# Optimization experiments

Measured on AMD Instinct MI355X. Metric: run time of the kernel, lower is better.

## Reference

```python
import jax, jax.numpy as jnp
import numpy as np

B, T, C = 2, 2048, 1024
N_HEADS = 16
HEAD_DIM = C // N_HEADS

def setup_inputs() -> dict:
    key = jax.random.key(0)
    k1, k2, k3 = jax.random.split(key, 3)
    x = jax.random.normal(k1, (B, T, C), dtype=jnp.float32)
    W_qkv = jax.random.normal(k2, (C, 3 * C), dtype=jnp.float32) * (1.0 / np.sqrt(C))
    W_out = jax.random.normal(k3, (C, C), dtype=jnp.float32) * (1.0 / np.sqrt(C))
    return {"x": x, "W_qkv": W_qkv, "W_out": W_out}

def reference(x, W_qkv, W_out):
    b, t, c = x.shape
    qkv = jnp.einsum('btc,cd->btd', x, W_qkv)  # [B,T,3C]
    q, k, v = jnp.split(qkv, 3, axis=-1)
    # [B, H, T, hd]
    q = q.reshape(b, t, N_HEADS, HEAD_DIM).transpose(0, 2, 1, 3)
    k = k.reshape(b, t, N_HEADS, HEAD_DIM).transpose(0, 2, 1, 3)
    v = v.reshape(b, t, N_HEADS, HEAD_DIM).transpose(0, 2, 1, 3)
    scale = 1.0 / jnp.sqrt(jnp.asarray(HEAD_DIM, dtype=x.dtype))
    attn = jnp.einsum('bhqd,bhkd->bhqk', q, k) * scale  # [B,H,T,T]
    causal = jnp.tril(jnp.ones((t, t), dtype=bool))
    attn = jnp.where(causal, attn, jnp.asarray(-1e9, dtype=attn.dtype))
    attn = jax.nn.softmax(attn, axis=-1)
    out = jnp.einsum('bhqk,bhkd->bhqd', attn, v)
    out = out.transpose(0, 2, 1, 3).reshape(b, t, c)
    return jnp.einsum('btc,cd->btd', out, W_out)
```

## Files before the change

### kernel.cpp

```cpp
#include <hip/hip_runtime.h>
#include <hip/hip_bf16.h>

typedef __attribute__((ext_vector_type(8))) short short8;
typedef __attribute__((ext_vector_type(4))) short bf16x4;
typedef __attribute__((ext_vector_type(4))) float floatx4;

#define T_SEQ 2048
#define NH    16
#define HD    64
#define QSCALE 0.18033688f

#define MFMA16(a, b, c) __builtin_amdgcn_mfma_f32_16x16x16bf16_1k(a, b, c, 0, 0, 0)
#define MFMA32(a, b, c) __builtin_amdgcn_mfma_f32_16x16x32_bf16(a, b, c, 0, 0, 0)

__device__ __forceinline__ ushort f2bf(float f) {
    union { float f; unsigned u; } un; un.f = f;
    unsigned r = un.u + 0x7fff + ((un.u >> 16) & 1);
    return (ushort)(r >> 16);
}
__device__ __forceinline__ unsigned pkbf(float a, float b) {
    __hip_bfloat162 t = __float22bfloat162_rn(float2{a, b});
    return *reinterpret_cast<unsigned*>(&t);
}

typedef const __attribute__((address_space(1))) unsigned int* gp1_t;
typedef __attribute__((address_space(3))) unsigned int* lp3_t;
__device__ __forceinline__ void gl_lds16(const ushort* g, ushort* l) {
    __builtin_amdgcn_global_load_lds((gp1_t)g, (lp3_t)l, 16, 0, 0);
}

__global__ void prep_kernel(const float* __restrict__ Wqkv, const float* __restrict__ Wout,
                            const float* __restrict__ x, ushort* __restrict__ wt_qkv,
                            ushort* __restrict__ wt_out, ushort* __restrict__ x_bf) {
    __shared__ ushort tile[32][33];
    const int bid = blockIdx.x;
    if (bid >= 4096) {
        size_t i = ((size_t)(bid - 4096) * 256 + threadIdx.x) * 8;
        float4 f0 = *(const float4*)(x + i);
        float4 f1 = *(const float4*)(x + i + 4);
        short8 v;
        v[0] = (short)f2bf(f0.x); v[1] = (short)f2bf(f0.y);
        v[2] = (short)f2bf(f0.z); v[3] = (short)f2bf(f0.w);
        v[4] = (short)f2bf(f1.x); v[5] = (short)f2bf(f1.y);
        v[6] = (short)f2bf(f1.z); v[7] = (short)f2bf(f1.w);
        *(short8*)(x_bf + i) = v;
        return;
    }
    const float* in; ushort* out; int R, C, gx, gy;
    if (bid < 3072) { in = Wqkv; out = wt_qkv; R = 1024; C = 3072; gx = bid % 96; gy = bid / 96; }
    else            { int t = bid - 3072; in = Wout; out = wt_out; R = 1024; C = 1024; gx = t & 31; gy = t >> 5; }
    const int tx = threadIdx.x & 31, ty = threadIdx.x >> 5;
    const int bx = gx * 32, by = gy * 32;
    #pragma unroll
    for (int i = ty; i < 32; i += 8)
        tile[i][tx] = f2bf(in[(size_t)(by + i) * C + bx + tx]);
    __syncthreads();
    #pragma unroll
    for (int i = ty; i < 32; i += 8)
        out[(size_t)(bx + i) * R + by + tx] = tile[tx][i];
}

template <int EPI, int BN, int CM, int CN>
__global__ __launch_bounds__(256, 3)
void gemm_bt(const ushort* __restrict__ A, const ushort* __restrict__ Bt,
             void* __restrict__ O0, ushort* __restrict__ O1, ushort* __restrict__ O2,
             int M, int N, int K) {
    constexpr int NJ = BN / 32;
    constexpr int NB = (BN * 8) / 256;
    __shared__ __align__(16) ushort smem[8192 + BN * 64];
    ushort* As = smem;
    ushort* Bs = smem + 8192;
    const int tid  = threadIdx.x;
    const int wave = tid >> 6, lane = tid & 63;
    const int quad = lane >> 4, l16 = lane & 15;
    const int wm = (wave >> 1) * 64, wn = (wave & 1) * (BN / 2);

    const int lid = blockIdx.y * gridDim.x + blockIdx.x;
    const int xcd = lid & 7, ib = lid >> 3;
    const int NGY = (int)gridDim.y / CN;
    const int m0 = ((xcd / NGY) * CM + ib / CN) * 128;
    const int n0 = ((xcd % NGY) * CN + ib % CN) * BN;

    const ushort* aP[4];
    const ushort* bP[NB];
    #pragma unroll
    for (int j = 0; j < 4; j++) {
        int c = tid + j * 256;
        int r = c >> 3;
        int g = ((c & 7) ^ (r & 7)) * 8;
        aP[j] = A + (size_t)(m0 + r) * K + g;
    }
    #pragma unroll
    for (int j = 0; j < NB; j++) {
        int c = tid + j * 256;
        int r = c >> 3;
        int g = ((c & 7) ^ (r & 7)) * 8;
        bP[j] = Bt + (size_t)(n0 + r) * K + g;
    }

    floatx4 acc[4][NJ];
    #pragma unroll
    for (int i = 0; i < 4; i++)
        #pragma unroll
        for (int j = 0; j < NJ; j++)
            acc[i][j] = (floatx4){0.f, 0.f, 0.f, 0.f};

    const int xsw = l16 & 7;

    for (int k0 = 0; k0 < K; k0 += 64) {
        __syncthreads();
        #pragma unroll
        for (int j = 0; j < 4; j++)  gl_lds16(aP[j] + k0, &As[(tid + j * 256) * 8]);
        #pragma unroll
        for (int j = 0; j < NB; j++) gl_lds16(bP[j] + k0, &Bs[(tid + j * 256) * 8]);
        __syncthreads();
        #pragma unroll
        for (int kk = 0; kk < 2; kk++) {
            short8 af[4], bf[NJ];
            #pragma unroll
            for (int i = 0; i < 4; i++)
                af[i] = *(const short8*)(&As[(wm + i * 16 + l16) * 64 + ((kk * 4 + quad) ^ xsw) * 8]);
            #pragma unroll
            for (int j = 0; j < NJ; j++)
                bf[j] = *(const short8*)(&Bs[(wn + j * 16 + l16) * 64 + ((kk * 4 + quad) ^ xsw) * 8]);
            #pragma unroll
            for (int i = 0; i < 4; i++)
                #pragma unroll
                for (int j = 0; j < NJ; j++)
                    acc[i][j] = MFMA32(af[i], bf[j], acc[i][j]);
        }
    }

    if constexpr (EPI == 0) {
        const int b = m0 >> 11;
        const int t0 = m0 & 2047;
        if (n0 >= 2048) {
            const int head0 = (n0 - 2048) >> 6;
            __syncthreads();
            #pragma unroll
            for (int nh = 0; nh < 2; nh++) {
                if ((wave & 1) == nh) {
                    #pragma unroll
                    for (int j = 0; j < NJ; j++)
                        #pragma unroll
                        for (int i = 0; i < 4; i++) {
                            int nl = j * 16 + l16;
                            int mB = wm + i * 16 + quad * 4;
                            *(unsigned*)(&smem[nl * 136 + mB])     = pkbf(acc[i][j][0], acc[i][j][1]);
                            *(unsigned*)(&smem[nl * 136 + mB + 2]) = pkbf(acc[i][j][2], acc[i][j][3]);
                        }
                }
                __syncthreads();
                #pragma unroll
                for (int cc = 0; cc < 4; cc++) {
                    int c = cc * 256 + tid;
                    int row = c >> 4, mcol = (c & 15) * 8;
                    uint4 v = *(const uint4*)(&smem[row * 136 + mcol]);
                    *(uint4*)(&O2[((size_t)(b * NH + head0 + nh) * HD + row) * T_SEQ + t0 + mcol]) = v;
                }
                __syncthreads();
            }
        } else {
            __syncthreads();
            #pragma unroll
            for (int nh = 0; nh < 2; nh++) {
                const int nn = n0 + nh * 64;
                const int part = nn >> 10;
                const int head = (nn & 1023) >> 6;
                ushort* OP = (part == 0) ? (ushort*)O0 : O1;
                const float qs = (part == 0) ? QSCALE : 1.0f;
                if ((wave & 1) == nh) {
                    #pragma unroll
                    for (int i = 0; i < 4; i++)
                        #pragma unroll
                        for (int j = 0; j < NJ; j++) {
                            const int col = j * 16 + l16;
                            const int rowb = wm + i * 16 + quad * 4;
                            #pragma unroll
                            for (int r = 0; r < 4; r++)
                                smem[(rowb + r) * 72 + col] = f2bf(acc[i][j][r] * qs);
                        }
                }
                __syncthreads();
                const size_t obase = ((size_t)(b * NH + head)) * T_SEQ + t0;
                #pragma unroll
                for (int cc = 0; cc < 4; cc++) {
                    int c = cc * 256 + tid;
                    int row = c >> 3, col8 = (c & 7) * 8;
                    uint4 v = *(const uint4*)(&smem[row * 72 + col8]);
                    *(uint4*)(&OP[(obase + row) * HD + col8]) = v;
                }
                __syncthreads();
            }
        }
        return;
    } else {
        #pragma unroll
        for (int i = 0; i < 4; i++)
            #pragma unroll
            for (int j = 0; j < NJ; j++)
                #pragma unroll
                for (int r = 0; r < 4; r++) {
                    int m = m0 + wm + i * 16 + quad * 4 + r;
                    int n = n0 + wn + j * 16 + l16;
                    ((float*)O0)[(size_t)m * N + n] = acc[i][j][r];
                }
    }
}

__device__ __forceinline__ void softmax_step(floatx4 s[4], float& mst, float& ll,
                                             floatx4 o[4], bf16x4 pf[4]) {
    float t0 = fmaxf(fmaxf(s[0][0], s[0][1]), fmaxf(s[0][2], s[0][3]));
    float t1 = fmaxf(fmaxf(s[1][0], s[1][1]), fmaxf(s[1][2], s[1][3]));
    float t2 = fmaxf(fmaxf(s[2][0], s[2][1]), fmaxf(s[2][2], s[2][3]));
    float t3 = fmaxf(fmaxf(s[3][0], s[3][1]), fmaxf(s[3][2], s[3][3]));
    float t  = fmaxf(fmaxf(t0, t1), fmaxf(t2, t3));
    if (!__all(t - mst <= 8.0f)) {
        t = fmaxf(t, __shfl_xor(t, 16));
        t = fmaxf(t, __shfl_xor(t, 32));
        float mnew  = fmaxf(mst, t);
        float alpha = exp2f(mst - mnew);
        mst = mnew;
        ll  *= alpha;
        #pragma unroll
        for (int db = 0; db < 4; db++)
            #pragma unroll
            for (int r = 0; r < 4; r++) o[db][r] *= alpha;
    }
    #pragma unroll
    for (int j = 0; j < 4; j++) {
        float p0 = exp2f(s[j][0] - mst);
        float p1 = exp2f(s[j][1] - mst);
        float p2 = exp2f(s[j][2] - mst);
        float p3 = exp2f(s[j][3] - mst);
        ll += (p0 + p1) + (p2 + p3);
        union { bf16x4 v; unsigned u[2]; } pu;
        pu.u[0] = pkbf(p0, p1);
        pu.u[1] = pkbf(p2, p3);
        pf[j] = pu.v;
    }
}

__global__ __launch_bounds__(256, 2)
void attn_kernel(const ushort* __restrict__ Q, const ushort* __restrict__ Kk,
                 const ushort* __restrict__ Vt, ushort* __restrict__ Oout) {
    __shared__ __align__(16) ushort Ks[2][128 * 64];
    __shared__ __align__(16) ushort Vs[2][64 * 128];
    const int tid  = threadIdx.x;
    const int wave = tid >> 6, lane = tid & 63;
    const int quad = lane >> 4, l16 = lane & 15;
    const int idx = blockIdx.x;
    const int bh = idx & 31;
    const int jp = idx >> 5;
    const int p  = (jp < 8) ? jp : (15 - (jp - 8));
    const int qtA = p, qtB = 31 - p;
    const int b = bh >> 4, h = bh & 15;

    const ushort* qp = Q  + (size_t)bh * T_SEQ * HD;
    const ushort* kp = Kk + (size_t)bh * T_SEQ * HD;
    const ushort* vp = Vt + (size_t)bh * HD * T_SEQ;

    const int q0A = qtA * 64 + wave * 16;
    const int q0B = qtB * 64 + wave * 16;

    short8 qfA[2], qfB[2];
    #pragma unroll
    for (int kb = 0; kb < 2; kb++) {
        qfA[kb] = *(const short8*)(qp + (size_t)(q0A + l16) * HD + kb * 32 + quad * 8);
        qfB[kb] = *(const short8*)(qp + (size_t)(q0B + l16) * HD + kb * 32 + quad * 8);
    }

    floatx4 oA[4], oB[4];
    #pragma unroll
    for (int db = 0; db < 4; db++) {
        oA[db] = (floatx4){0.f, 0.f, 0.f, 0.f};
        oB[db] = (floatx4){0.f, 0.f, 0.f, 0.f};
    }
    float mA = -1e30f, llA = 0.f, mB = -1e30f, llB = 0.f;

    int koff[4], voff[4];
    #pragma unroll
    for (int j = 0; j < 4; j++) {
        int c = tid + j * 256;
        int kr = c >> 3;
        koff[j] = kr * HD + (((c & 7) ^ (kr & 7)) * 8);
        int vr = c >> 4;
        voff[j] = vr * T_SEQ + ((((c & 15) ^ (vr & 7))) * 8);
    }

#define STAGE(BUF, I)                                                            \
    {                                                                            \
        const ushort* kg = kp + (size_t)(I) * 128 * HD;                          \
        const ushort* vg = vp + (I) * 128;                                       \
        gl_lds16(kg + koff[0], &Ks[BUF][(tid      ) * 8]);                       \
        gl_lds16(kg + koff[1], &Ks[BUF][(tid + 256) * 8]);                       \
        gl_lds16(kg + koff[2], &Ks[BUF][(tid + 512) * 8]);                       \
        gl_lds16(kg + koff[3], &Ks[BUF][(tid + 768) * 8]);                       \
        gl_lds16(vg + voff[0], &Vs[BUF][(tid      ) * 8]);                       \
        gl_lds16(vg + voff[1], &Vs[BUF][(tid + 256) * 8]);                       \
        gl_lds16(vg + voff[2], &Vs[BUF][(tid + 512) * 8]);                       \
        gl_lds16(vg + voff[3], &Vs[BUF][(tid + 768) * 8]);                       \
    }

    const int xsw = (l16 & 7), qh = quad >> 1, ql = quad & 1;
    const int ka0 = l16 * 64 + ((quad ^ xsw) * 8);
    const int ka1 = l16 * 64 + (((4 + quad) ^ xsw) * 8);
    int va[4];
    #pragma unroll
    for (int jj = 0; jj < 4; jj++)
        va[jj] = l16 * 128 + (((2 * jj + qh) ^ xsw) * 8) + ql * 4;

#define ZS(S) { _Pragma("unroll") for (int z = 0; z < 4; z++) S[z] = (floatx4){0.f, 0.f, 0.f, 0.f}; }

#define QKD(SB, SA, BUF, ST)                                                     \
    {                                                                            \
        _Pragma("unroll")                                                        \
        for (int jj = 0; jj < 4; jj++) {                                         \
            short8 kf = *(const short8*)(&Ks[BUF][(ST) * 4096 + jj * 1024 + ka0]); \
            SB[jj] = MFMA32(kf, qfB[0], SB[jj]);                                 \
            SA[jj] = MFMA32(kf, qfA[0], SA[jj]);                                 \
        }                                                                        \
        _Pragma("unroll")                                                        \
        for (int jj = 0; jj < 4; jj++) {                                         \
            short8 kf = *(const short8*)(&Ks[BUF][(ST) * 4096 + jj * 1024 + ka1]); \
            SB[jj] = MFMA32(kf, qfB[1], SB[jj]);                                 \
            SA[jj] = MFMA32(kf, qfA[1], SA[jj]);                                 \
        }                                                                        \
    }

#define QK1(SB, BUF, ST)                                                         \
    {                                                                            \
        _Pragma("unroll")                                                        \
        for (int jj = 0; jj < 4; jj++) {                                         \
            short8 kf = *(const short8*)(&Ks[BUF][(ST) * 4096 + jj * 1024 + ka0]); \
            SB[jj] = MFMA32(kf, qfB[0], SB[jj]);                                 \
        }                                                                        \
        _Pragma("unroll")                                                        \
        for (int jj = 0; jj < 4; jj++) {                                         \
            short8 kf = *(const short8*)(&Ks[BUF][(ST) * 4096 + jj * 1024 + ka1]); \
            SB[jj] = MFMA32(kf, qfB[1], SB[jj]);                                 \
        }                                                                        \
    }

#define MASKD(S)                                                                 \
    {                                                                            \
        _Pragma("unroll")                                                        \
        for (int jj = 0; jj < 4; jj++)                                           \
            _Pragma("unroll")                                                    \
            for (int rr = 0; rr < 4; rr++)                                       \
                if (jj * 16 + quad * 4 + rr > wave * 16 + l16) S[jj][rr] = -1e30f; \
    }

#define PVG(O, PF, BUF, ST)                                                      \
    {                                                                            \
        _Pragma("unroll")                                                        \
        for (int jj = 0; jj < 4; jj++)                                           \
            _Pragma("unroll")                                                    \
            for (int db = 0; db < 4; db++) {                                     \
                bf16x4 vf = *(const bf16x4*)(&Vs[BUF][va[jj] + (ST) * 64 + db * 2048]); \
                O[db] = MFMA16(vf, PF[jj], O[db]);                               \
            }                                                                    \
    }

#define ITER(BUF, I)                                                             \
    {                                                                            \
        __syncthreads();                                                         \
        if ((I) + 1 < NT) STAGE((BUF) ^ 1, (I) + 1)                              \
        const int kt0 = 2 * (I), kt1 = kt0 + 1;                                  \
        const bool v1 = (kt1 <= qtB);                                            \
        const bool a0 = (kt0 <= qtA), a1 = (kt1 <= qtA);                         \
        floatx4 sB0[4], sB1[4], sA0[4], sA1[4];                                  \
        bf16x4 pfB0[4], pfB1[4], pfA0[4], pfA1[4];                               \
        __builtin_amdgcn_s_setprio(1);                                           \
        ZS(sB0)                                                                  \
        if (a0) { ZS(sA0) QKD(sB0, sA0, BUF, 0) } else { QK1(sB0, BUF, 0) }      \
        if (v1) {                                                                \
            ZS(sB1)                                                              \
            if (a1) { ZS(sA1) QKD(sB1, sA1, BUF, 1) } else { QK1(sB1, BUF, 1) }  \
        }                                                                        \
        __builtin_amdgcn_s_setprio(0);                                           \
        if (kt0 == qtB) { MASKD(sB0) }                                           \
        if (v1 && kt1 == qtB) { MASKD(sB1) }                                     \
        if (a0 && kt0 == qtA) { MASKD(sA0) }                                     \
        if (a1 && kt1 == qtA) { MASKD(sA1) }                                     \
        softmax_step(sB0, mB, llB, oB, pfB0);                                    \
        PVG(oB, pfB0, BUF, 0)                                                    \
        if (v1) { softmax_step(sB1, mB, llB, oB, pfB1); PVG(oB, pfB1, BUF, 1) }  \
        if (a0) { softmax_step(sA0, mA, llA, oA, pfA0); PVG(oA, pfA0, BUF, 0) }  \
        if (a1) { softmax_step(sA1, mA, llA, oA, pfA1); PVG(oA, pfA1, BUF, 1) }  \
    }

    const int NT = (qtB + 2) >> 1;
    STAGE(0, 0)

    int i = 0;
    for (; i + 1 < NT; i += 2) {
        ITER(0, i)
        ITER(1, i + 1)
    }
    if (i < NT) ITER(0, i)
#undef ITER
#undef PVG
#undef MASKD
#undef QK1
#undef QKD
#undef ZS
#undef STAGE

    {
        float lB = llB;
        lB += __shfl_xor(lB, 16);
        lB += __shfl_xor(lB, 32);
        const float inv = 1.0f / lB;
        const int t = q0B + l16;
        #pragma unroll
        for (int db = 0; db < 4; db++) {
            union { ushort4 w; unsigned u[2]; } ou;
            ou.u[0] = pkbf(oB[db][0] * inv, oB[db][1] * inv);
            ou.u[1] = pkbf(oB[db][2] * inv, oB[db][3] * inv);
            *(ushort4*)(Oout + (((size_t)b * T_SEQ + t) * NH + h) * HD + db * 16 + quad * 4) = ou.w;
        }
    }
    {
        float lA = llA;
        lA += __shfl_xor(lA, 16);
        lA += __shfl_xor(lA, 32);
        const float inv = 1.0f / lA;
        const int t = q0A + l16;
        #pragma unroll
        for (int db = 0; db < 4; db++) {
            union { ushort4 w; unsigned u[2]; } ou;
            ou.u[0] = pkbf(oA[db][0] * inv, oA[db][1] * inv);
            ou.u[1] = pkbf(oA[db][2] * inv, oA[db][3] * inv);
            *(ushort4*)(Oout + (((size_t)b * T_SEQ + t) * NH + h) * HD + db * 16 + quad * 4) = ou.w;
        }
    }
}

extern "C" void kernel_launch(void* const* d_in, const int* in_sizes, int n_in,
                              void* d_out, int out_size, void* d_ws, size_t ws_size,
                              hipStream_t stream) {
    const float* x    = (const float*)d_in[0];
    const float* Wqkv = (const float*)d_in[1];
    const float* Wout = (const float*)d_in[2];
    ushort* ws = (ushort*)d_ws;

    ushort* wt_qkv = ws;
    ushort* wt_out = wt_qkv + 3072 * 1024;
    ushort* q_ws   = wt_out + 1024 * 1024;
    ushort* k_ws   = q_ws + 4194304;
    ushort* v_t    = k_ws + 4194304;
    ushort* a_out  = v_t + 4194304;
    ushort* x_bf   = a_out + 4194304;

    prep_kernel<<<dim3(6144), 256, 0, stream>>>(Wqkv, Wout, x, wt_qkv, wt_out, x_bf);

    gemm_bt<0, 128, 8, 12><<<dim3(32, 24), 256, 0, stream>>>(x_bf, wt_qkv, q_ws, k_ws, v_t,
                                                             4096, 3072, 1024);

    attn_kernel<<<dim3(512), 256, 0, stream>>>(q_ws, k_ws, v_t, a_out);

    gemm_bt<1, 64, 4, 16><<<dim3(32, 16), 256, 0, stream>>>(a_out, wt_out, (float*)d_out,
                                                            nullptr, nullptr, 4096, 1024, 1024);
}
```

Baseline: 169.6 us.

## Double-buffer GEMM LDS tiles with K=32 stages to overlap loads and MFMA

Replaces the single-buffered K=64 LDS tile loop in the GEMM with a two-buffer pipeline of K=32 stages. The next stage's global-to-LDS load is issued before computing on the current buffer, and the XOR swizzle is adapted to the 32-wide rows. The aim is to hide global load latency behind MFMA work at the same LDS footprint. The trade-off is twice as many barriers per K, and the epilogue's reuse of smem must still fit the new layout.

```diff
diff --git a/kernel.cpp b/kernel.cpp
--- a/kernel.cpp
+++ b/kernel.cpp
@@ -65,11 +65,13 @@
 void gemm_bt(const ushort* __restrict__ A, const ushort* __restrict__ Bt,
              void* __restrict__ O0, ushort* __restrict__ O1, ushort* __restrict__ O2,
              int M, int N, int K) {
-    constexpr int NJ = BN / 32;
-    constexpr int NB = (BN * 8) / 256;
-    __shared__ __align__(16) ushort smem[8192 + BN * 64];
+    constexpr int NJ   = BN / 32;
+    constexpr int NBCH = BN / 64;
+    constexpr int ABUF = 128 * 32;
+    constexpr int BBUF = BN * 32;
+    __shared__ __align__(16) ushort smem[2 * ABUF + 2 * BBUF];
     ushort* As = smem;
-    ushort* Bs = smem + 8192;
+    ushort* Bs = smem + 2 * ABUF;
     const int tid  = threadIdx.x;
     const int wave = tid >> 6, lane = tid & 63;
     const int quad = lane >> 4, l16 = lane & 15;
@@ -81,20 +83,20 @@
     const int m0 = ((xcd / NGY) * CM + ib / CN) * 128;
     const int n0 = ((xcd % NGY) * CN + ib % CN) * BN;
 
-    const ushort* aP[4];
-    const ushort* bP[NB];
-    #pragma unroll
-    for (int j = 0; j < 4; j++) {
+    const ushort* aP[2];
+    #pragma unroll
+    for (int j = 0; j < 2; j++) {
         int c = tid + j * 256;
-        int r = c >> 3;
-        int g = ((c & 7) ^ (r & 7)) * 8;
+        int r = c >> 2;
+        int g = ((c & 3) ^ ((r >> 1) & 3)) * 8;
         aP[j] = A + (size_t)(m0 + r) * K + g;
     }
-    #pragma unroll
-    for (int j = 0; j < NB; j++) {
+    const ushort* bP[NBCH];
+    #pragma unroll
+    for (int j = 0; j < NBCH; j++) {
         int c = tid + j * 256;
-        int r = c >> 3;
-        int g = ((c & 7) ^ (r & 7)) * 8;
+        int r = c >> 2;
+        int g = ((c & 3) ^ ((r >> 1) & 3)) * 8;
         bP[j] = Bt + (size_t)(n0 + r) * K + g;
     }
 
@@ -105,31 +107,46 @@
         for (int j = 0; j < NJ; j++)
             acc[i][j] = (floatx4){0.f, 0.f, 0.f, 0.f};
 
-    const int xsw = l16 & 7;
-
-    for (int k0 = 0; k0 < K; k0 += 64) {
+    const int col_sw = (quad ^ ((l16 >> 1) & 3)) * 8;
+
+#define GSTAGE(B, S)                                                             \
+    {                                                                            \
+        const size_t ko = (size_t)(S) * 32;                                      \
+        gl_lds16(aP[0] + ko, &As[(B) * ABUF + tid * 8]);                         \
+        gl_lds16(aP[1] + ko, &As[(B) * ABUF + (tid + 256) * 8]);                 \
+        _Pragma("unroll")                                                        \
+        for (int j = 0; j < NBCH; j++)                                           \
+            gl_lds16(bP[j] + ko, &Bs[(B) * BBUF + (tid + j * 256) * 8]);         \
+    }
+
+#define GCOMP(B)                                                                 \
+    {                                                                            \
+        short8 af[4], bf[NJ];                                                    \
+        _Pragma("unroll")                                                        \
+        for (int i = 0; i < 4; i++)                                              \
+            af[i] = *(const short8*)(&As[(B) * ABUF + (wm + i * 16 + l16) * 32 + col_sw]); \
+        _Pragma("unroll")                                                        \
+        for (int j = 0; j < NJ; j++)                                             \
+            bf[j] = *(const short8*)(&Bs[(B) * BBUF + (wn + j * 16 + l16) * 32 + col_sw]); \
+        _Pragma("unroll")                                                        \
+        for (int i = 0; i < 4; i++)                                              \
+            _Pragma("unroll")                                                    \
+            for (int j = 0; j < NJ; j++)                                         \
+                acc[i][j] = MFMA32(af[i], bf[j], acc[i][j]);                     \
+    }
+
+    const int NS = K >> 5;
+    GSTAGE(0, 0)
+    for (int s = 0; s < NS; s += 2) {
         __syncthreads();
-        #pragma unroll
-        for (int j = 0; j < 4; j++)  gl_lds16(aP[j] + k0, &As[(tid + j * 256) * 8]);
-        #pragma unroll
-        for (int j = 0; j < NB; j++) gl_lds16(bP[j] + k0, &Bs[(tid + j * 256) * 8]);
+        if (s + 1 < NS) GSTAGE(1, s + 1)
+        GCOMP(0)
         __syncthreads();
-        #pragma unroll
-        for (int kk = 0; kk < 2; kk++) {
-            short8 af[4], bf[NJ];
-            #pragma unroll
-            for (int i = 0; i < 4; i++)
-                af[i] = *(const short8*)(&As[(wm + i * 16 + l16) * 64 + ((kk * 4 + quad) ^ xsw) * 8]);
-            #pragma unroll
-            for (int j = 0; j < NJ; j++)
-                bf[j] = *(const short8*)(&Bs[(wn + j * 16 + l16) * 64 + ((kk * 4 + quad) ^ xsw) * 8]);
-            #pragma unroll
-            for (int i = 0; i < 4; i++)
-                #pragma unroll
-                for (int j = 0; j < NJ; j++)
-                    acc[i][j] = MFMA32(af[i], bf[j], acc[i][j]);
-        }
-    }
+        if (s + 2 < NS) GSTAGE(0, s + 2)
+        GCOMP(1)
+    }
+#undef GCOMP
+#undef GSTAGE
 
     if constexpr (EPI == 0) {
         const int b = m0 >> 11;
```

New measurement: 173.7 us. 2.4% more time.
